# Performance work log

Measured on AMD Instinct MI355X. Metric: run time of the kernel, lower is better.

Reference implementation:

```python
import jax, jax.numpy as jnp
import numpy as np

N, E = 50000, 800000
IN_CH, H, C = 256, 8, 32
HID = H * C  # 256, equals IN_CH so no residual projection
T = 2  # n_edge_types
FFN = 4 * HID
EPS = 1e-5


def setup_inputs() -> dict:
    key = jax.random.key(0)
    ks = jax.random.split(key, 16)
    s_in = 1.0 / np.sqrt(IN_CH)
    s_h = 1.0 / np.sqrt(HID)
    return {
        "x": jax.random.normal(ks[0], (N, IN_CH), jnp.float32),
        "edge_index": jax.random.randint(ks[1], (2, E), 0, N, jnp.int32),
        "edge_type": jax.random.randint(ks[2], (E,), 0, T, jnp.int32),
        "edge_weight": jax.random.uniform(ks[3], (E,), jnp.float32),
        "W_src": jax.random.normal(ks[4], (H * C, IN_CH), jnp.float32) * s_in,
        "W_dst": jax.random.normal(ks[5], (H * C, IN_CH), jnp.float32) * s_in,
        "att_src": jax.random.normal(ks[6], (T, H, C), jnp.float32) * (1.0 / np.sqrt(C)),
        "att_dst": jax.random.normal(ks[7], (T, H, C), jnp.float32) * (1.0 / np.sqrt(C)),
        "bias": jnp.zeros((HID,), jnp.float32),
        "ln1_g": jnp.ones((HID,), jnp.float32),
        "ln1_b": jnp.zeros((HID,), jnp.float32),
        "ln2_g": jnp.ones((HID,), jnp.float32),
        "ln2_b": jnp.zeros((HID,), jnp.float32),
        "ffn_W1": jax.random.normal(ks[8], (FFN, HID), jnp.float32) * s_h,
        "ffn_b1": jnp.zeros((FFN,), jnp.float32),
        "ffn_W2": jax.random.normal(ks[9], (HID, FFN), jnp.float32) * (1.0 / np.sqrt(FFN)),
        "ffn_b2": jnp.zeros((HID,), jnp.float32),
    }


def _layernorm(h, g, b):
    mu = jnp.mean(h, axis=-1, keepdims=True)
    var = jnp.mean(jnp.square(h - mu), axis=-1, keepdims=True)
    return (h - mu) * jax.lax.rsqrt(var + EPS) * g + b


def _gat_forward(x, edge_index, edge_type, edge_weight, W_src, W_dst,
                 att_src, att_dst, bias, ln1_g, ln1_b, ln2_g, ln2_b,
                 ffn_W1, ffn_b1, ffn_W2, ffn_b2):
    n = x.shape[0]
    # add self-loops (type 0, weight 1)
    loop = jnp.arange(n, dtype=edge_index.dtype)
    src = jnp.concatenate([edge_index[0], loop])
    dst = jnp.concatenate([edge_index[1], loop])
    etype = jnp.concatenate([edge_type, jnp.zeros((n,), edge_type.dtype)])
    ew = jnp.concatenate([edge_weight, jnp.ones((n,), edge_weight.dtype)])

    x_src = (x @ W_src.T).reshape(n, H, C)
    x_dst = (x @ W_dst.T).reshape(n, H, C)

    xs_j = x_src[src]            # [Et,H,C] gathered source feats
    xd_i = x_dst[dst]            # [Et,H,C] gathered dest feats
    a_s = att_src[etype]         # [Et,H,C]
    a_d = att_dst[etype]
    alpha = jnp.sum(xs_j * a_s, axis=-1) + jnp.sum(xd_i * a_d, axis=-1)  # [Et,H]
    alpha = jnp.where(alpha >= 0, alpha, 0.2 * alpha)  # leaky_relu(0.2)

    # segment softmax over destination node per head
    m = jax.lax.stop_gradient(jax.ops.segment_max(alpha, dst, num_segments=n))
    a = jnp.exp(alpha - m[dst])
    denom = jax.ops.segment_sum(a, dst, num_segments=n)
    a = a / denom[dst]
    a = a * ew[:, None]          # edge weights (self-loops weight 1)

    msg = xs_j * a[:, :, None]   # [Et,H,C]
    out = jax.ops.segment_sum(msg, dst, num_segments=n)  # [n,H,C]
    out = out.reshape(n, H * C) + bias

    h = _layernorm(out + x, ln1_g, ln1_b)  # residual (in == hidden)
    ff = jax.nn.gelu(h @ ffn_W1.T + ffn_b1, approximate=False) @ ffn_W2.T + ffn_b2
    return _layernorm(h + ff, ln2_g, ln2_b)


def reference(x, edge_index, edge_type, edge_weight, W_src, W_dst,
              att_src, att_dst, bias, ln1_g, ln1_b, ln2_g, ln2_b,
              ffn_W1, ffn_b1, ffn_W2, ffn_b2):
    return _gat_forward(x, edge_index, edge_type, edge_weight, W_src, W_dst,
                        att_src, att_dst, bias, ln1_g, ln1_b, ln2_g, ln2_b,
                        ffn_W1, ffn_b1, ffn_W2, ffn_b2)
```

## Files before the change

### kernel.cpp

```cpp
#include <hip/hip_runtime.h>

typedef unsigned short u16;
typedef unsigned int u32;
typedef __attribute__((ext_vector_type(8))) unsigned short ushort8v;
typedef __attribute__((ext_vector_type(8))) __bf16 bf16x8;
typedef __attribute__((ext_vector_type(4))) float f32x4;

__device__ __forceinline__ float bf2f(u16 u) { return __uint_as_float(((u32)u) << 16); }
__device__ __forceinline__ u16 f2bf(float f) {
    u32 u = __float_as_uint(f);
    u32 r = u + 0x7fffu + ((u >> 16) & 1u);
    return (u16)(r >> 16);
}
__device__ __forceinline__ float wave_sum(float v) {
    #pragma unroll
    for (int m = 1; m < 64; m <<= 1) v += __shfl_xor(v, m, 64);
    return v;
}
__device__ __forceinline__ float gld(const void* p, size_t i, bool f32) {
    return f32 ? ((const float*)p)[i] : bf2f(((const u16*)p)[i]);
}
__device__ __forceinline__ void gst(void* p, size_t i, bool f32, float v) {
    if (f32) ((float*)p)[i] = v;
    else     ((u16*)p)[i] = f2bf(v);
}
__device__ __forceinline__ void ldf8(const void* p, size_t i, bool f32, float* o) {
    if (f32) {
        const float4* q = (const float4*)((const float*)p + i);
        float4 a = q[0], b = q[1];
        o[0] = a.x; o[1] = a.y; o[2] = a.z; o[3] = a.w;
        o[4] = b.x; o[5] = b.y; o[6] = b.z; o[7] = b.w;
    } else {
        ushort8v v = *(const ushort8v*)((const u16*)p + i);
        #pragma unroll
        for (int j = 0; j < 8; j++) o[j] = bf2f(v[j]);
    }
}
__device__ __forceinline__ void gl2lds16(const u16* g, u16* l) {
    __builtin_amdgcn_global_load_lds((const __attribute__((address_space(1))) void*)g,
                                     (__attribute__((address_space(3))) void*)l, 16, 0, 0);
}
__device__ __forceinline__ float gelu_f(float v) {
    float ay = fabsf(v) * 0.70710678f;
    float t = __builtin_amdgcn_rcpf(1.0f + 0.47047f * ay);
    float poly = t * (0.3480242f + t * (-0.0958798f + t * 0.7478556f));
    float erfa = 1.0f - poly * __expf(-ay * ay);
    float er = (v >= 0.f) ? erfa : -erfa;
    return 0.5f * v * (1.0f + er);
}

__global__ void __launch_bounds__(256) k_probe(const u16* __restrict__ x, u32* __restrict__ flag) {
    __shared__ int cnt;
    if (threadIdx.x == 0) cnt = 0;
    __syncthreads();
    int bad = 0;
    for (int i = threadIdx.x; i < 2048; i += 256) {
        float v = bf2f(x[i]);
        if (!(v > -64.f && v < 64.f)) bad = 1;
    }
    if (bad) atomicAdd(&cnt, 1);
    __syncthreads();
    if (threadIdx.x == 0) flag[0] = (cnt > 0) ? 1u : 0u;
}

__global__ void __launch_bounds__(256) k_zero(u32* __restrict__ p, int n) {
    int i = blockIdx.x * 256 + threadIdx.x;
    if (i < n) p[i] = 0u;
}

__global__ void __launch_bounds__(256) k_cvt(const u32* __restrict__ dflag,
                                             const void* __restrict__ src, u16* __restrict__ dst, int n8) {
    bool f32 = dflag[0] != 0u;
    int i = blockIdx.x * 256 + threadIdx.x;
    if (i >= n8) return;
    float t[8];
    ldf8(src, (size_t)i * 8, f32, t);
    ushort8v o;
    #pragma unroll
    for (int j = 0; j < 8; j++) o[j] = f2bf(t[j]);
    *(ushort8v*)&dst[(size_t)i * 8] = o;
}

template <int EPI>
__global__ void __launch_bounds__(256, 5) mgemm4(const u32* __restrict__ dflag,
                                                 const u16* __restrict__ A, const u16* __restrict__ B,
                                                 void* __restrict__ Cout, const void* __restrict__ bias,
                                                 int M, int Nn, int K, int ldC, int arow0) {
    const bool ibf32 = dflag[0] != 0u;
    __shared__ __attribute__((aligned(16))) u16 sA[2][128 * 32];
    __shared__ __attribute__((aligned(16))) u16 sB[2][128 * 32];

    int nwg = gridDim.x * gridDim.y;
    int wgid = blockIdx.y * gridDim.x + blockIdx.x;
    if (nwg >= 16) {
        int q = nwg >> 3, r = nwg & 7;
        int xcd = wgid & 7, i = wgid >> 3;
        wgid = (xcd < r ? xcd * (q + 1) : r * (q + 1) + (xcd - r) * q) + i;
    }
    const int m0 = (wgid / gridDim.x) * 128;
    const int n0 = (wgid % gridDim.x) * 128;

    const int tid = threadIdx.x;
    const int wid = tid >> 6;
    const int lane = tid & 63;

    const int wm = (wid >> 1) * 64;
    const int wn = (wid & 1) * 64;
    const int lr = lane & 15;
    const int kg = lane >> 4;
    const int gsw = (kg ^ ((lr >> 1) & 3)) * 8;

    const int srow = lane >> 2;
    const int scol = ((lane & 3) ^ ((lane >> 3) & 3)) * 8;

    f32x4 acc[4][4] = {};

    const size_t abase = (size_t)arow0 * K;

    {
        #pragma unroll
        for (int j = 0; j < 2; j++) {
            int u = wid * 2 + j;
            int gr = m0 + u * 16 + srow; if (gr >= M) gr = M - 1;
            gl2lds16(A + abase + (size_t)gr * K + scol, &sA[0][u * 512]);
        }
        #pragma unroll
        for (int j = 0; j < 2; j++) {
            int u = wid * 2 + j;
            int gr = n0 + u * 16 + srow; if (gr >= Nn) gr = Nn - 1;
            gl2lds16(B + (size_t)gr * K + scol, &sB[0][u * 512]);
        }
    }
    __syncthreads();

    int cur = 0;
    for (int k0 = 0; k0 < K; k0 += 32) {
        if (k0 + 32 < K) {
            int nb = cur ^ 1, k1 = k0 + 32;
            #pragma unroll
            for (int j = 0; j < 2; j++) {
                int u = wid * 2 + j;
                int gr = m0 + u * 16 + srow; if (gr >= M) gr = M - 1;
                gl2lds16(A + abase + (size_t)gr * K + k1 + scol, &sA[nb][u * 512]);
            }
            #pragma unroll
            for (int j = 0; j < 2; j++) {
                int u = wid * 2 + j;
                int gr = n0 + u * 16 + srow; if (gr >= Nn) gr = Nn - 1;
                gl2lds16(B + (size_t)gr * K + k1 + scol, &sB[nb][u * 512]);
            }
        }
        {
            bf16x8 afr[4], bfr[4];
            #pragma unroll
            for (int m = 0; m < 4; m++)
                afr[m] = __builtin_bit_cast(bf16x8, *(const ushort8v*)&sA[cur][(wm + m * 16 + lr) * 32 + gsw]);
            #pragma unroll
            for (int n = 0; n < 4; n++)
                bfr[n] = __builtin_bit_cast(bf16x8, *(const ushort8v*)&sB[cur][(wn + n * 16 + lr) * 32 + gsw]);
            #pragma unroll
            for (int m = 0; m < 4; m++)
                #pragma unroll
                for (int n = 0; n < 4; n++)
                    acc[m][n] = __builtin_amdgcn_mfma_f32_16x16x32_bf16(afr[m], bfr[n], acc[m][n], 0, 0, 0);
        }
        __syncthreads();
        cur ^= 1;
    }

    float bv[4];
    if (EPI == 1) {
        #pragma unroll
        for (int n = 0; n < 4; n++) {
            int cn = n0 + wn + n * 16 + lr; if (cn >= Nn) cn = Nn - 1;
            bv[n] = gld(bias, cn, ibf32);
        }
    }
    const int or0 = (lane >> 4) << 2;
    #pragma unroll
    for (int m = 0; m < 4; m++) {
        #pragma unroll
        for (int r = 0; r < 4; r++) {
            int gr = m0 + wm + m * 16 + or0 + r;
            if (gr >= M) continue;
            #pragma unroll
            for (int n = 0; n < 4; n++) {
                int cn = n0 + wn + n * 16 + lr;
                if (cn >= Nn) continue;
                float v = acc[m][n][r];
                if (EPI == 1) {
                    ((u16*)Cout)[(size_t)gr * ldC + cn] = f2bf(gelu_f(v + bv[n]));
                } else if (EPI == 0) {
                    ((u16*)Cout)[(size_t)gr * ldC + cn] = f2bf(v);
                } else {
                    ((float*)Cout)[(size_t)gr * ldC + cn] = v;
                }
            }
        }
    }
}

__global__ void __launch_bounds__(256) k_mkatt(const u32* __restrict__ dflag,
                                               const void* __restrict__ Wsrc, const void* __restrict__ Wdst,
                                               const void* __restrict__ attS, const void* __restrict__ attD,
                                               u16* __restrict__ Mmat, int K) {
    bool f32 = dflag[0] != 0u;
    int th = blockIdx.x;
    int k = threadIdx.x;
    int tt = th & 15;
    const void* W = (th < 16) ? Wsrc : Wdst;
    const void* att = (th < 16) ? attS : attD;
    int h = tt & 7;
    float s = 0.f;
    #pragma unroll 8
    for (int c = 0; c < 32; c++)
        s += gld(W, (size_t)(h * 32 + c) * K + k, f32) * gld(att, tt * 32 + c, f32);
    Mmat[th * K + k] = f2bf(s);
}

__global__ void __launch_bounds__(256) k_count(const int* __restrict__ ei, u32* __restrict__ cnt, int E) {
    int e = blockIdx.x * 256 + threadIdx.x;
    if (e < E) atomicAdd(cnt + ei[E + e], 1u);
}
__global__ void __launch_bounds__(256) k_scanA(u32* __restrict__ buf, u32* __restrict__ bsum, int N) {
    int t = threadIdx.x, idx = blockIdx.x * 256 + t;
    u32 v = (idx < N) ? buf[idx] : 0u;
    __shared__ u32 sc[256];
    sc[t] = v; __syncthreads();
    for (int d = 1; d < 256; d <<= 1) {
        u32 add = (t >= d) ? sc[t - d] : 0u; __syncthreads();
        sc[t] += add; __syncthreads();
    }
    if (idx < N) buf[idx] = sc[t] - v;
    if (t == 255) bsum[blockIdx.x] = sc[255];
}
__global__ void __launch_bounds__(256) k_scanB(u32* __restrict__ bsum, int nb) {
    int t = threadIdx.x;
    u32 v = (t < nb) ? bsum[t] : 0u;
    __shared__ u32 sc[256];
    sc[t] = v; __syncthreads();
    for (int d = 1; d < 256; d <<= 1) {
        u32 add = (t >= d) ? sc[t - d] : 0u; __syncthreads();
        sc[t] += add; __syncthreads();
    }
    if (t < nb) bsum[t] = sc[t] - v;
}
__global__ void __launch_bounds__(256) k_scanC(u32* __restrict__ obuf, u32* __restrict__ cursor,
                                               const u32* __restrict__ bsum, int N, int E) {
    int idx = blockIdx.x * 256 + threadIdx.x;
    if (idx < N) {
        u32 o = obuf[idx] + bsum[blockIdx.x];
        obuf[idx] = o;
        cursor[idx] = o;
    }
    if (blockIdx.x == 0 && threadIdx.x == 0) obuf[N] = (u32)E;
}
__global__ void __launch_bounds__(256) k_scatter(const int* __restrict__ ei, u32* __restrict__ cursor,
                                                 u32* __restrict__ elist, int E) {
    int e = blockIdx.x * 256 + threadIdx.x;
    if (e >= E) return;
    u32 slot = atomicAdd(cursor + ei[E + e], 1u);
    elist[slot] = (u32)e;
}

__global__ void __launch_bounds__(256) k_node(const u32* __restrict__ dflag,
                                              const int* __restrict__ ei, const int* __restrict__ et,
                                              const void* __restrict__ ew, const void* __restrict__ x,
                                              const u16* __restrict__ xsd,
                                              const u32* __restrict__ obuf, const u32* __restrict__ elist,
                                              const void* __restrict__ bias,
                                              const void* __restrict__ g1, const void* __restrict__ b1,
                                              void* __restrict__ hout, u16* __restrict__ hb, int N) {
    bool f32 = dflag[0] != 0u;
    const int wid = threadIdx.x >> 6;
    const int lane = threadIdx.x & 63;
    const int node = blockIdx.x * 4 + wid;
    if (node >= N) return;

    __shared__ u32 s_src[4][64];
    __shared__ float s_w[4][64];
    __shared__ float s_pe[4][64][8];

    const int ch0 = lane * 4;
    const int hh = lane >> 3;
    const size_t nbase = (size_t)node * 288;

    ushort8v dd0v = *(const ushort8v*)&xsd[nbase + 256 + 16];
    ushort8v dd1v = *(const ushort8v*)&xsd[nbase + 256 + 24];

    float a_self = bf2f(xsd[nbase + 256 + hh]) + bf2f(xsd[nbase + 256 + 16 + hh]);
    float p_self = __expf(a_self >= 0.f ? a_self : 0.2f * a_self);
    float den = p_self;
    ushort4 sv = *(const ushort4*)&xsd[nbase + ch0];
    float num0 = p_self * bf2f(sv.x), num1 = p_self * bf2f(sv.y);
    float num2 = p_self * bf2f(sv.z), num3 = p_self * bf2f(sv.w);

    const u32 kbeg = obuf[node], kend = obuf[node + 1];
    for (u32 c0 = kbeg; c0 < kend; c0 += 64) {
        int cnt = (int)(kend - c0) < 64 ? (int)(kend - c0) : 64;
        __builtin_amdgcn_wave_barrier();
        if (lane < cnt) {
            int e = (int)elist[c0 + lane];
            int src = ei[e];
            int t = et[e];
            s_src[wid][lane] = (u32)src;
            s_w[wid][lane] = gld(ew, e, f32);
            ushort8v ds8 = *(const ushort8v*)&xsd[(size_t)src * 288 + 256 + t * 8];
            #pragma unroll
            for (int h = 0; h < 8; h++) {
                float aa = bf2f(ds8[h]) + (t ? bf2f(dd1v[h]) : bf2f(dd0v[h]));
                s_pe[wid][lane][h] = __expf(aa >= 0.f ? aa : 0.2f * aa);
            }
        }
        __builtin_amdgcn_wave_barrier();
        int k = 0;
        for (; k + 4 <= cnt; k += 4) {
            u32 sa = s_src[wid][k], sb = s_src[wid][k + 1];
            u32 sc = s_src[wid][k + 2], sd = s_src[wid][k + 3];
            float pa = s_pe[wid][k][hh], pb = s_pe[wid][k + 1][hh];
            float pc = s_pe[wid][k + 2][hh], pd = s_pe[wid][k + 3][hh];
            float wa = s_w[wid][k], wb = s_w[wid][k + 1];
            float wc = s_w[wid][k + 2], wd = s_w[wid][k + 3];
            ushort4 xa = *(const ushort4*)&xsd[(size_t)sa * 288 + ch0];
            ushort4 xb = *(const ushort4*)&xsd[(size_t)sb * 288 + ch0];
            ushort4 xc = *(const ushort4*)&xsd[(size_t)sc * 288 + ch0];
            ushort4 xd = *(const ushort4*)&xsd[(size_t)sd * 288 + ch0];
            float pwa = pa * wa, pwb = pb * wb, pwc = pc * wc, pwd = pd * wd;
            num0 += pwa * bf2f(xa.x) + pwb * bf2f(xb.x) + pwc * bf2f(xc.x) + pwd * bf2f(xd.x);
            num1 += pwa * bf2f(xa.y) + pwb * bf2f(xb.y) + pwc * bf2f(xc.y) + pwd * bf2f(xd.y);
            num2 += pwa * bf2f(xa.z) + pwb * bf2f(xb.z) + pwc * bf2f(xc.z) + pwd * bf2f(xd.z);
            num3 += pwa * bf2f(xa.w) + pwb * bf2f(xb.w) + pwc * bf2f(xc.w) + pwd * bf2f(xd.w);
            den += (pa + pb) + (pc + pd);
        }
        for (; k < cnt; k++) {
            u32 s = s_src[wid][k];
            float p = s_pe[wid][k][hh];
            float pw = p * s_w[wid][k];
            ushort4 xv = *(const ushort4*)&xsd[(size_t)s * 288 + ch0];
            num0 += pw * bf2f(xv.x); num1 += pw * bf2f(xv.y);
            num2 += pw * bf2f(xv.z); num3 += pw * bf2f(xv.w);
            den += p;
        }
    }

    float rden = 1.0f / den;
    float xr0, xr1, xr2, xr3;
    if (f32) {
        float4 t = *(const float4*)((const float*)x + (size_t)node * 256 + ch0);
        xr0 = t.x; xr1 = t.y; xr2 = t.z; xr3 = t.w;
    } else {
        ushort4 t = *(const ushort4*)((const u16*)x + (size_t)node * 256 + ch0);
        xr0 = bf2f(t.x); xr1 = bf2f(t.y); xr2 = bf2f(t.z); xr3 = bf2f(t.w);
    }
    float v0 = num0 * rden + gld(bias, ch0 + 0, f32) + xr0;
    float v1 = num1 * rden + gld(bias, ch0 + 1, f32) + xr1;
    float v2 = num2 * rden + gld(bias, ch0 + 2, f32) + xr2;
    float v3 = num3 * rden + gld(bias, ch0 + 3, f32) + xr3;

    float mu = wave_sum(v0 + v1 + v2 + v3) * (1.f / 256.f);
    float d0 = v0 - mu, d1 = v1 - mu, d2 = v2 - mu, d3 = v3 - mu;
    float var = wave_sum(d0 * d0 + d1 * d1 + d2 * d2 + d3 * d3) * (1.f / 256.f);
    float rs = rsqrtf(var + 1e-5f);
    float o0 = d0 * rs * gld(g1, ch0 + 0, f32) + gld(b1, ch0 + 0, f32);
    float o1 = d1 * rs * gld(g1, ch0 + 1, f32) + gld(b1, ch0 + 1, f32);
    float o2 = d2 * rs * gld(g1, ch0 + 2, f32) + gld(b1, ch0 + 2, f32);
    float o3 = d3 * rs * gld(g1, ch0 + 3, f32) + gld(b1, ch0 + 3, f32);

    size_t base = (size_t)node * 256 + ch0;
    gst(hout, base + 0, f32, o0); gst(hout, base + 1, f32, o1);
    gst(hout, base + 2, f32, o2); gst(hout, base + 3, f32, o3);
    ushort4 hv; hv.x = f2bf(o0); hv.y = f2bf(o1); hv.z = f2bf(o2); hv.w = f2bf(o3);
    *(ushort4*)&hb[base] = hv;
}

__global__ void __launch_bounds__(256) k_ln2(const u32* __restrict__ dflag,
                                             void* __restrict__ h, int row0, const u16* __restrict__ ffn,
                                             const void* __restrict__ fb2, const void* __restrict__ g,
                                             const void* __restrict__ b, int rows) {
    bool f32 = dflag[0] != 0u;
    int row = blockIdx.x * 4 + (threadIdx.x >> 6);
    if (row >= rows) return;
    int lane = threadIdx.x & 63;
    size_t hbase = (size_t)(row0 + row) * 256 + lane * 4;
    size_t fbase = (size_t)row * 256 + lane * 4;
    ushort4 tv = *(const ushort4*)(ffn + fbase);
    float v0 = bf2f(tv.x) + gld(h, hbase + 0, f32) + gld(fb2, lane * 4 + 0, f32);
    float v1 = bf2f(tv.y) + gld(h, hbase + 1, f32) + gld(fb2, lane * 4 + 1, f32);
    float v2 = bf2f(tv.z) + gld(h, hbase + 2, f32) + gld(fb2, lane * 4 + 2, f32);
    float v3 = bf2f(tv.w) + gld(h, hbase + 3, f32) + gld(fb2, lane * 4 + 3, f32);
    float mu = wave_sum(v0 + v1 + v2 + v3) * (1.f / 256.f);
    float d0 = v0 - mu, d1 = v1 - mu, d2 = v2 - mu, d3 = v3 - mu;
    float var = wave_sum(d0 * d0 + d1 * d1 + d2 * d2 + d3 * d3) * (1.f / 256.f);
    float rs = rsqrtf(var + 1e-5f);
    gst(h, hbase + 0, f32, d0 * rs * gld(g, lane * 4 + 0, f32) + gld(b, lane * 4 + 0, f32));
    gst(h, hbase + 1, f32, d1 * rs * gld(g, lane * 4 + 1, f32) + gld(b, lane * 4 + 1, f32));
    gst(h, hbase + 2, f32, d2 * rs * gld(g, lane * 4 + 2, f32) + gld(b, lane * 4 + 2, f32));
    gst(h, hbase + 3, f32, d3 * rs * gld(g, lane * 4 + 3, f32) + gld(b, lane * 4 + 3, f32));
}

extern "C" void kernel_launch(void* const* d_in, const int* in_sizes, int n_in,
                              void* d_out, int out_size, void* d_ws, size_t ws_size,
                              hipStream_t stream) {
    const int N = in_sizes[0] / 256;
    const int E = in_sizes[1] / 2;
    const int NB = (N + 255) / 256;

    const void* x    = d_in[0];
    const int*  ei   = (const int*)d_in[1];
    const int*  et   = (const int*)d_in[2];
    const void* ew   = d_in[3];
    const void* Wsrc = d_in[4];
    const void* Wdst = d_in[5];
    const void* attS = d_in[6];
    const void* attD = d_in[7];
    const void* bias = d_in[8];
    const void* g1   = d_in[9];
    const void* b1   = d_in[10];
    const void* g2   = d_in[11];
    const void* b2   = d_in[12];
    const void* W1   = d_in[13];
    const void* fb1  = d_in[14];
    const void* W2   = d_in[15];
    const void* fb2  = d_in[16];

    char* ws = (char*)d_ws;
    u32* flag   = (u32*)(ws + 0);
    u32* bsum   = (u32*)(ws + 256);
    u32* obuf   = (u32*)(ws + 1536);
    u32* cursor = (u32*)(ws + 201984);
    u32* elist  = (u32*)(ws + 402176);
    u16* xb     = (u16*)(ws + 3602176);
    u16* hb     = (u16*)(ws + 3602176);
    u16* xsd    = (u16*)(ws + 29202176);
    u16* Bcat   = (u16*)(ws + 58002176);
    u16* W1b    = (u16*)(ws + 58149632);
    u16* W2b    = (u16*)(ws + 58673920);
    char* ffnbuf = ws + 59198208;
    void* hbuf  = d_out;

    k_probe<<<1, 256, 0, stream>>>((const u16*)x, flag);

    k_cvt<<<(N * 32 + 255) / 256, 256, 0, stream>>>(flag, x, xb, N * 32);
    k_cvt<<<32, 256, 0, stream>>>(flag, Wsrc, Bcat, 8192);
    k_cvt<<<128, 256, 0, stream>>>(flag, W1, W1b, 32768);
    k_cvt<<<128, 256, 0, stream>>>(flag, W2, W2b, 32768);
    k_mkatt<<<32, 256, 0, stream>>>(flag, Wsrc, Wdst, attS, attD, Bcat + 256 * 256, 256);

    const int gyN = (N + 127) / 128;

    mgemm4<0><<<dim3(3, gyN), 256, 0, stream>>>(flag, xb, Bcat, xsd, nullptr, N, 288, 256, 288, 0);

    k_zero<<<NB, 256, 0, stream>>>(obuf, N);
    k_count<<<(E + 255) / 256, 256, 0, stream>>>(ei, obuf, E);
    k_scanA<<<NB, 256, 0, stream>>>(obuf, bsum, N);
    k_scanB<<<1, 256, 0, stream>>>(bsum, NB);
    k_scanC<<<NB, 256, 0, stream>>>(obuf, cursor, bsum, N, E);
    k_scatter<<<(E + 255) / 256, 256, 0, stream>>>(ei, cursor, elist, E);

    k_node<<<(N + 3) / 4, 256, 0, stream>>>(flag, ei, et, ew, x, xsd, obuf, elist,
                                            bias, g1, b1, hbuf, hb, N);

    long long avail = (long long)ws_size - 59198208 - 256;
    int rc = (int)(avail / 2560);
    rc &= ~127;
    if (rc > 50048) rc = 50048;
    if (rc < 128) rc = 128;
    u16* act    = (u16*)ffnbuf;
    u16* ffnout = (u16*)(ffnbuf + (size_t)rc * 2048);

    for (int r0 = 0; r0 < N; r0 += rc) {
        int rows = N - r0; if (rows > rc) rows = rc;
        int gy = (rows + 127) / 128;
        mgemm4<1><<<dim3(8, gy), 256, 0, stream>>>(flag, hb, W1b, act, fb1, rows, 1024, 256, 1024, r0);
        mgemm4<0><<<dim3(2, gy), 256, 0, stream>>>(flag, act, W2b, ffnout, nullptr, rows, 256, 1024, 256, 0);
        k_ln2<<<(rows + 3) / 4, 256, 0, stream>>>(flag, hbuf, r0, ffnout, fb2, g2, b2, rows);
    }
}
```

Before: 621.4 us.

## Fuse FFN second GEMM with LayerNorm2 and pack edge data during scatter

Adds a new GEMM kernel that computes the FFN down-projection over full 256-column rows per 64-row block. Its epilogue adds bias and residual and applies LayerNorm2, which removes the intermediate ffnout buffer and the separate k_ln2 launch. The scatter step now writes packed (src|type, weight) records in CSR order, so the node kernel no longer does indirect loads of edge_index, edge_type and edge_weight through elist. The node gather loop is also unrolled by 8 to keep more loads in flight. Risks: the fused GEMM has lower parallelism (one block per 64 rows) and variance computed as E[x^2]-mu^2, and pedge now shares the ffnbuf workspace region, which depends on pedge being consumed before act is written.

```diff
diff --git a/kernel.cpp b/kernel.cpp
--- a/kernel.cpp
+++ b/kernel.cpp
@@ -190,11 +190,150 @@
                 float v = acc[m][n][r];
                 if (EPI == 1) {
                     ((u16*)Cout)[(size_t)gr * ldC + cn] = f2bf(gelu_f(v + bv[n]));
-                } else if (EPI == 0) {
+                } else {
                     ((u16*)Cout)[(size_t)gr * ldC + cn] = f2bf(v);
-                } else {
-                    ((float*)Cout)[(size_t)gr * ldC + cn] = v;
                 }
+            }
+        }
+    }
+}
+
+__global__ void __launch_bounds__(256, 3) mgemm5(const u32* __restrict__ dflag,
+                                                 const u16* __restrict__ A, const u16* __restrict__ B,
+                                                 void* __restrict__ hout,
+                                                 const void* __restrict__ fb2, const void* __restrict__ g2,
+                                                 const void* __restrict__ b2, int M, int r0) {
+    const bool f32 = dflag[0] != 0u;
+    constexpr int K = 1024;
+    __shared__ __attribute__((aligned(16))) u16 sA[2][64 * 32];
+    __shared__ __attribute__((aligned(16))) u16 sB[2][256 * 32];
+    __shared__ float red[4][64][2];
+
+    int nwg = gridDim.x;
+    int wgid = blockIdx.x;
+    if (nwg >= 16) {
+        int q = nwg >> 3, r = nwg & 7;
+        int xcd = wgid & 7, i = wgid >> 3;
+        wgid = (xcd < r ? xcd * (q + 1) : r * (q + 1) + (xcd - r) * q) + i;
+    }
+    const int m0 = wgid * 64;
+
+    const int tid = threadIdx.x;
+    const int wid = tid >> 6;
+    const int lane = tid & 63;
+    const int lr = lane & 15;
+    const int kg = lane >> 4;
+    const int gsw = (kg ^ ((lr >> 1) & 3)) * 8;
+    const int srow = lane >> 2;
+    const int scol = ((lane & 3) ^ ((lane >> 3) & 3)) * 8;
+
+    f32x4 acc[4][4] = {};
+
+    {
+        int gr = m0 + wid * 16 + srow; if (gr >= M) gr = M - 1;
+        gl2lds16(A + (size_t)gr * K + scol, &sA[0][wid * 512]);
+        #pragma unroll
+        for (int j = 0; j < 4; j++) {
+            int u = wid * 4 + j;
+            gl2lds16(B + (size_t)(u * 16 + srow) * K + scol, &sB[0][u * 512]);
+        }
+    }
+    __syncthreads();
+
+    int cur = 0;
+    for (int k0 = 0; k0 < K; k0 += 32) {
+        if (k0 + 32 < K) {
+            int nb = cur ^ 1, k1 = k0 + 32;
+            int gr = m0 + wid * 16 + srow; if (gr >= M) gr = M - 1;
+            gl2lds16(A + (size_t)gr * K + k1 + scol, &sA[nb][wid * 512]);
+            #pragma unroll
+            for (int j = 0; j < 4; j++) {
+                int u = wid * 4 + j;
+                gl2lds16(B + (size_t)(u * 16 + srow) * K + k1 + scol, &sB[nb][u * 512]);
+            }
+        }
+        {
+            bf16x8 afr[4], bfr[4];
+            #pragma unroll
+            for (int m = 0; m < 4; m++)
+                afr[m] = __builtin_bit_cast(bf16x8, *(const ushort8v*)&sA[cur][(m * 16 + lr) * 32 + gsw]);
+            #pragma unroll
+            for (int n = 0; n < 4; n++)
+                bfr[n] = __builtin_bit_cast(bf16x8, *(const ushort8v*)&sB[cur][(wid * 64 + n * 16 + lr) * 32 + gsw]);
+            #pragma unroll
+            for (int m = 0; m < 4; m++)
+                #pragma unroll
+                for (int n = 0; n < 4; n++)
+                    acc[m][n] = __builtin_amdgcn_mfma_f32_16x16x32_bf16(afr[m], bfr[n], acc[m][n], 0, 0, 0);
+        }
+        __syncthreads();
+        cur ^= 1;
+    }
+
+    float fb[4], gg[4], bb[4];
+    #pragma unroll
+    for (int n = 0; n < 4; n++) {
+        int cn = wid * 64 + n * 16 + lr;
+        fb[n] = gld(fb2, cn, f32); gg[n] = gld(g2, cn, f32); bb[n] = gld(b2, cn, f32);
+    }
+    const int or0 = (lane >> 4) << 2;
+    float s1[4][4], s2[4][4];
+    #pragma unroll
+    for (int m = 0; m < 4; m++) {
+        #pragma unroll
+        for (int r = 0; r < 4; r++) {
+            int grow = m * 16 + or0 + r;
+            float a1 = 0.f, a2 = 0.f;
+            if (m0 + grow < M) {
+                #pragma unroll
+                for (int n = 0; n < 4; n++) {
+                    int cn = wid * 64 + n * 16 + lr;
+                    float hv = gld(hout, (size_t)(r0 + m0 + grow) * 256 + cn, f32);
+                    float v = acc[m][n][r] + hv + fb[n];
+                    acc[m][n][r] = v;
+                    a1 += v; a2 += v * v;
+                }
+            }
+            s1[m][r] = a1; s2[m][r] = a2;
+        }
+    }
+    #pragma unroll
+    for (int m = 0; m < 4; m++)
+        #pragma unroll
+        for (int r = 0; r < 4; r++) {
+            #pragma unroll
+            for (int d = 1; d < 16; d <<= 1) {
+                s1[m][r] += __shfl_xor(s1[m][r], d, 64);
+                s2[m][r] += __shfl_xor(s2[m][r], d, 64);
+            }
+        }
+    if (lr == 0) {
+        #pragma unroll
+        for (int m = 0; m < 4; m++)
+            #pragma unroll
+            for (int r = 0; r < 4; r++) {
+                int grow = m * 16 + or0 + r;
+                red[wid][grow][0] = s1[m][r];
+                red[wid][grow][1] = s2[m][r];
+            }
+    }
+    __syncthreads();
+    #pragma unroll
+    for (int m = 0; m < 4; m++) {
+        #pragma unroll
+        for (int r = 0; r < 4; r++) {
+            int grow = m * 16 + or0 + r;
+            if (m0 + grow >= M) continue;
+            float t1 = red[0][grow][0] + red[1][grow][0] + red[2][grow][0] + red[3][grow][0];
+            float t2 = red[0][grow][1] + red[1][grow][1] + red[2][grow][1] + red[3][grow][1];
+            float mu = t1 * (1.f / 256.f);
+            float var = fmaxf(t2 * (1.f / 256.f) - mu * mu, 0.f);
+            float rs = rsqrtf(var + 1e-5f);
+            #pragma unroll
+            for (int n = 0; n < 4; n++) {
+                int cn = wid * 64 + n * 16 + lr;
+                float o = (acc[m][n][r] - mu) * rs * gg[n] + bb[n];
+                gst(hout, (size_t)(r0 + m0 + grow) * 256 + cn, f32, o);
             }
         }
     }
@@ -255,19 +394,24 @@
     }
     if (blockIdx.x == 0 && threadIdx.x == 0) obuf[N] = (u32)E;
 }
-__global__ void __launch_bounds__(256) k_scatter(const int* __restrict__ ei, u32* __restrict__ cursor,
-                                                 u32* __restrict__ elist, int E) {
+__global__ void __launch_bounds__(256) k_scatter(const u32* __restrict__ dflag,
+                                                 const int* __restrict__ ei, const int* __restrict__ et,
+                                                 const void* __restrict__ ew, u32* __restrict__ cursor,
+                                                 uint2* __restrict__ pedge, int E) {
+    bool f32 = dflag[0] != 0u;
     int e = blockIdx.x * 256 + threadIdx.x;
     if (e >= E) return;
     u32 slot = atomicAdd(cursor + ei[E + e], 1u);
-    elist[slot] = (u32)e;
+    uint2 pk;
+    pk.x = (u32)ei[e] | ((u32)et[e] << 31);
+    pk.y = __float_as_uint(gld(ew, e, f32));
+    pedge[slot] = pk;
 }
 
 __global__ void __launch_bounds__(256) k_node(const u32* __restrict__ dflag,
-                                              const int* __restrict__ ei, const int* __restrict__ et,
-                                              const void* __restrict__ ew, const void* __restrict__ x,
+                                              const uint2* __restrict__ pedge, const void* __restrict__ x,
                                               const u16* __restrict__ xsd,
-                                              const u32* __restrict__ obuf, const u32* __restrict__ elist,
+                                              const u32* __restrict__ obuf,
                                               const void* __restrict__ bias,
                                               const void* __restrict__ g1, const void* __restrict__ b1,
                                               void* __restrict__ hout, u16* __restrict__ hb, int N) {
@@ -300,37 +444,58 @@
         int cnt = (int)(kend - c0) < 64 ? (int)(kend - c0) : 64;
         __builtin_amdgcn_wave_barrier();
         if (lane < cnt) {
-            int e = (int)elist[c0 + lane];
-            int src = ei[e];
-            int t = et[e];
-            s_src[wid][lane] = (u32)src;
-            s_w[wid][lane] = gld(ew, e, f32);
+            uint2 pe = pedge[c0 + lane];
+            u32 src = pe.x & 0x7fffffffu;
+            int t = (int)(pe.x >> 31);
+            s_src[wid][lane] = src;
+            s_w[wid][lane] = __uint_as_float(pe.y);
             ushort8v ds8 = *(const ushort8v*)&xsd[(size_t)src * 288 + 256 + t * 8];
+            ushort8v ddv = t ? dd1v : dd0v;
             #pragma unroll
             for (int h = 0; h < 8; h++) {
-                float aa = bf2f(ds8[h]) + (t ? bf2f(dd1v[h]) : bf2f(dd0v[h]));
+                float aa = bf2f(ds8[h]) + bf2f(ddv[h]);
                 s_pe[wid][lane][h] = __expf(aa >= 0.f ? aa : 0.2f * aa);
             }
         }
         __builtin_amdgcn_wave_barrier();
         int k = 0;
+        for (; k + 8 <= cnt; k += 8) {
+            u32 ss[8]; float pp[8], ww[8]; ushort4 gv[8];
+            #pragma unroll
+            for (int j = 0; j < 8; j++) {
+                ss[j] = s_src[wid][k + j];
+                pp[j] = s_pe[wid][k + j][hh];
+                ww[j] = s_w[wid][k + j];
+            }
+            #pragma unroll
+            for (int j = 0; j < 8; j++)
+                gv[j] = *(const ushort4*)&xsd[(size_t)ss[j] * 288 + ch0];
+            #pragma unroll
+            for (int j = 0; j < 8; j++) {
+                float q = pp[j] * ww[j];
+                num0 += q * bf2f(gv[j].x); num1 += q * bf2f(gv[j].y);
+                num2 += q * bf2f(gv[j].z); num3 += q * bf2f(gv[j].w);
+                den += pp[j];
+            }
+        }
         for (; k + 4 <= cnt; k += 4) {
-            u32 sa = s_src[wid][k], sb = s_src[wid][k + 1];
-            u32 sc = s_src[wid][k + 2], sd = s_src[wid][k + 3];
-            float pa = s_pe[wid][k][hh], pb = s_pe[wid][k + 1][hh];
-            float pc = s_pe[wid][k + 2][hh], pd = s_pe[wid][k + 3][hh];
-            float wa = s_w[wid][k], wb = s_w[wid][k + 1];
-            float wc = s_w[wid][k + 2], wd = s_w[wid][k + 3];
-            ushort4 xa = *(const ushort4*)&xsd[(size_t)sa * 288 + ch0];
-            ushort4 xb = *(const ushort4*)&xsd[(size_t)sb * 288 + ch0];
-            ushort4 xc = *(const ushort4*)&xsd[(size_t)sc * 288 + ch0];
-            ushort4 xd = *(const ushort4*)&xsd[(size_t)sd * 288 + ch0];
-            float pwa = pa * wa, pwb = pb * wb, pwc = pc * wc, pwd = pd * wd;
-            num0 += pwa * bf2f(xa.x) + pwb * bf2f(xb.x) + pwc * bf2f(xc.x) + pwd * bf2f(xd.x);
-            num1 += pwa * bf2f(xa.y) + pwb * bf2f(xb.y) + pwc * bf2f(xc.y) + pwd * bf2f(xd.y);
-            num2 += pwa * bf2f(xa.z) + pwb * bf2f(xb.z) + pwc * bf2f(xc.z) + pwd * bf2f(xd.z);
-            num3 += pwa * bf2f(xa.w) + pwb * bf2f(xb.w) + pwc * bf2f(xc.w) + pwd * bf2f(xd.w);
-            den += (pa + pb) + (pc + pd);
+            u32 ss[4]; float pp[4], ww[4]; ushort4 gv[4];
+            #pragma unroll
+            for (int j = 0; j < 4; j++) {
+                ss[j] = s_src[wid][k + j];
+                pp[j] = s_pe[wid][k + j][hh];
+                ww[j] = s_w[wid][k + j];
+            }
+            #pragma unroll
+            for (int j = 0; j < 4; j++)
+                gv[j] = *(const ushort4*)&xsd[(size_t)ss[j] * 288 + ch0];
+            #pragma unroll
+            for (int j = 0; j < 4; j++) {
+                float q = pp[j] * ww[j];
+                num0 += q * bf2f(gv[j].x); num1 += q * bf2f(gv[j].y);
+                num2 += q * bf2f(gv[j].z); num3 += q * bf2f(gv[j].w);
+                den += pp[j];
+            }
         }
         for (; k < cnt; k++) {
             u32 s = s_src[wid][k];
@@ -371,31 +536,6 @@
     gst(hout, base + 2, f32, o2); gst(hout, base + 3, f32, o3);
     ushort4 hv; hv.x = f2bf(o0); hv.y = f2bf(o1); hv.z = f2bf(o2); hv.w = f2bf(o3);
     *(ushort4*)&hb[base] = hv;
-}
-
-__global__ void __launch_bounds__(256) k_ln2(const u32* __restrict__ dflag,
-                                             void* __restrict__ h, int row0, const u16* __restrict__ ffn,
-                                             const void* __restrict__ fb2, const void* __restrict__ g,
-                                             const void* __restrict__ b, int rows) {
-    bool f32 = dflag[0] != 0u;
-    int row = blockIdx.x * 4 + (threadIdx.x >> 6);
-    if (row >= rows) return;
-    int lane = threadIdx.x & 63;
-    size_t hbase = (size_t)(row0 + row) * 256 + lane * 4;
-    size_t fbase = (size_t)row * 256 + lane * 4;
-    ushort4 tv = *(const ushort4*)(ffn + fbase);
-    float v0 = bf2f(tv.x) + gld(h, hbase + 0, f32) + gld(fb2, lane * 4 + 0, f32);
-    float v1 = bf2f(tv.y) + gld(h, hbase + 1, f32) + gld(fb2, lane * 4 + 1, f32);
-    float v2 = bf2f(tv.z) + gld(h, hbase + 2, f32) + gld(fb2, lane * 4 + 2, f32);
-    float v3 = bf2f(tv.w) + gld(h, hbase + 3, f32) + gld(fb2, lane * 4 + 3, f32);
-    float mu = wave_sum(v0 + v1 + v2 + v3) * (1.f / 256.f);
-    float d0 = v0 - mu, d1 = v1 - mu, d2 = v2 - mu, d3 = v3 - mu;
-    float var = wave_sum(d0 * d0 + d1 * d1 + d2 * d2 + d3 * d3) * (1.f / 256.f);
-    float rs = rsqrtf(var + 1e-5f);
-    gst(h, hbase + 0, f32, d0 * rs * gld(g, lane * 4 + 0, f32) + gld(b, lane * 4 + 0, f32));
-    gst(h, hbase + 1, f32, d1 * rs * gld(g, lane * 4 + 1, f32) + gld(b, lane * 4 + 1, f32));
-    gst(h, hbase + 2, f32, d2 * rs * gld(g, lane * 4 + 2, f32) + gld(b, lane * 4 + 2, f32));
-    gst(h, hbase + 3, f32, d3 * rs * gld(g, lane * 4 + 3, f32) + gld(b, lane * 4 + 3, f32));
 }
 
 extern "C" void kernel_launch(void* const* d_in, const int* in_sizes, int n_in,
@@ -428,13 +568,13 @@
     u32* bsum   = (u32*)(ws + 256);
     u32* obuf   = (u32*)(ws + 1536);
     u32* cursor = (u32*)(ws + 201984);
-    u32* elist  = (u32*)(ws + 402176);
     u16* xb     = (u16*)(ws + 3602176);
     u16* hb     = (u16*)(ws + 3602176);
     u16* xsd    = (u16*)(ws + 29202176);
     u16* Bcat   = (u16*)(ws + 58002176);
     u16* W1b    = (u16*)(ws + 58149632);
     u16* W2b    = (u16*)(ws + 58673920);
+    uint2* pedge = (uint2*)(ws + 59198208);
     char* ffnbuf = ws + 59198208;
     void* hbuf  = d_out;
 
@@ -455,24 +595,23 @@
     k_scanA<<<NB, 256, 0, stream>>>(obuf, bsum, N);
     k_scanB<<<1, 256, 0, stream>>>(bsum, NB);
     k_scanC<<<NB, 256, 0, stream>>>(obuf, cursor, bsum, N, E);
-    k_scatter<<<(E + 255) / 256, 256, 0, stream>>>(ei, cursor, elist, E);
-
-    k_node<<<(N + 3) / 4, 256, 0, stream>>>(flag, ei, et, ew, x, xsd, obuf, elist,
+    k_scatter<<<(E + 255) / 256, 256, 0, stream>>>(flag, ei, et, ew, cursor, pedge, E);
+
+    k_node<<<(N + 3) / 4, 256, 0, stream>>>(flag, pedge, x, xsd, obuf,
                                             bias, g1, b1, hbuf, hb, N);
 
     long long avail = (long long)ws_size - 59198208 - 256;
-    int rc = (int)(avail / 2560);
+    int rc = (int)(avail / 2048);
     rc &= ~127;
     if (rc > 50048) rc = 50048;
     if (rc < 128) rc = 128;
-    u16* act    = (u16*)ffnbuf;
-    u16* ffnout = (u16*)(ffnbuf + (size_t)rc * 2048);
+    u16* act = (u16*)ffnbuf;
 
     for (int r0 = 0; r0 < N; r0 += rc) {
         int rows = N - r0; if (rows > rc) rows = rc;
         int gy = (rows + 127) / 128;
         mgemm4<1><<<dim3(8, gy), 256, 0, stream>>>(flag, hb, W1b, act, fb1, rows, 1024, 256, 1024, r0);
-        mgemm4<0><<<dim3(2, gy), 256, 0, stream>>>(flag, act, W2b, ffnout, nullptr, rows, 256, 1024, 256, 0);
-        k_ln2<<<(rows + 3) / 4, 256, 0, stream>>>(flag, hbuf, r0, ffnout, fb2, g2, b2, rows);
-    }
-}
+        int g5 = (rows + 63) / 64;
+        mgemm5<<<g5, 256, 0, stream>>>(flag, act, W2b, hbuf, fb2, g2, b2, rows, r0);
+    }
+}
```

Measured after the change: 560.5 us. -9.8%, faster.
